# Kernel optimization log

Measured on AMD Instinct MI355X. Metric: run time of the kernel, lower is better.

The kernel has to match this reference:

```python
import jax, jax.numpy as jnp
import numpy as np


def _hilbert_d2xy(n, d):
    # standard Hilbert curve: distance d -> (x, y) on n x n grid (n power of 2)
    x = y = 0
    t = d
    s = 1
    while s < n:
        rx = 1 & (t // 2)
        ry = 1 & (t ^ rx)
        if ry == 0:
            if rx == 1:
                x = s - 1 - x
                y = s - 1 - y
            x, y = y, x
        x += s * rx
        y += s * ry
        t //= 4
        s *= 2
    return x, y


def _hilbert_perm(seq_len):
    n = int(round(np.sqrt(seq_len)))
    assert n * n == seq_len
    perm = np.empty(seq_len, dtype=np.int32)
    for d in range(seq_len):
        x, y = _hilbert_d2xy(n, d)
        perm[d] = y * n + x  # linear (row-major) index visited at Hilbert step d
    return perm


def setup_inputs() -> dict:
    key = jax.random.key(0)
    k1, k2, k3 = jax.random.split(key, 3)
    B, S, H, D = 1, 4096, 8, 64
    q = jax.random.normal(k1, (B, S, H, D), dtype=jnp.float32)
    k = jax.random.normal(k2, (B, S, H, D), dtype=jnp.float32)
    v = jax.random.normal(k3, (B, S, H, D), dtype=jnp.float32)
    hilbert_perm = jnp.asarray(_hilbert_perm(S))
    return {"q": q, "k": k, "v": v, "hilbert_perm": hilbert_perm}


def reference(q, k, v, hilbert_perm):
    B, S, H, D = q.shape
    inv_perm = jnp.argsort(hilbert_perm)

    # apply_hilbert_ordering along dim=1 (seq): gather by permutation
    q_o = q[:, hilbert_perm]
    k_o = k[:, hilbert_perm]
    v_o = v[:, hilbert_perm]

    # faithful to original: raw flat reshape of [B,S,H,D] -> [B*H, S, D]
    q_f = q_o.reshape(B * H, S, D)
    k_f = k_o.reshape(B * H, S, D)
    v_f = v_o.reshape(B * H, S, D)

    scale = 1.0 / jnp.sqrt(jnp.asarray(D, dtype=q.dtype))
    scores = jnp.einsum('bsd,btd->bst', q_f, k_f) * scale  # [B*H, S, S]
    attn = jax.nn.softmax(scores, axis=-1)
    out_f = jnp.einsum('bst,btd->bsd', attn, v_f)  # [B*H, S, D]

    out = out_f.reshape(B, H, S, D).transpose(0, 2, 1, 3).reshape(B, S, H, D)
    # inverse Hilbert ordering along dim=1
    return out[:, inv_perm]
```

## Files before the change

kernel.cpp:

```cpp
#include <hip/hip_runtime.h>

typedef _Float16 f16;
typedef _Float16 f16x4 __attribute__((ext_vector_type(4)));
typedef _Float16 f16x8 __attribute__((ext_vector_type(8)));
typedef __fp16 fp16x2 __attribute__((ext_vector_type(2)));
typedef float f32x4 __attribute__((ext_vector_type(4)));

#define MFMA_16x16x32_F16(A, B, C) __builtin_amdgcn_mfma_f32_16x16x32_f16((A), (B), (C), 0, 0, 0)

typedef const __attribute__((address_space(1))) char gchar;
typedef __attribute__((address_space(3))) char lchar;

__device__ __forceinline__ float fexp2(float x) { return __builtin_amdgcn_exp2f(x); }
__device__ __forceinline__ int swzb(int b) { return b ^ ((b >> 3) & 0x70); }

namespace {
constexpr int SB = 4096;
constexpr size_t BB = (size_t)SB * 64 * 2;
}

__device__ __forceinline__ int kinv(int r) {
    return 32 * (r >> 5) + 8 * ((r >> 2) & 3) + 4 * ((r >> 4) & 1) + (r & 3);
}

__global__ __launch_bounds__(256)
void hilbert_prepass_kernel(const float* __restrict__ kp, const float* __restrict__ vp,
                            const int* __restrict__ perm,
                            char* __restrict__ kw, char* __restrict__ vtw)
{
    const int bid = blockIdx.x;
    const int batch = bid & 7;
    const int tile = bid >> 3;
    const int tid = (int)threadIdx.x;
    const int r = tid >> 2;
    const int c4 = tid & 3;

    __shared__ float Vl[64][68];

    const int t = tile * 64 + r;
    const int srow = perm[batch * 512 + (t >> 3)];
    const size_t boff = (size_t)srow * 512 + (t & 7) * 64 + c4 * 16;

    {
        const float* ks = kp + boff;
        const float4 k0 = *(const float4*)(ks + 0);
        const float4 k1 = *(const float4*)(ks + 4);
        const float4 k2 = *(const float4*)(ks + 8);
        const float4 k3 = *(const float4*)(ks + 12);
        f16x8 h0, h1;
        h0[0] = (f16)k0.x; h0[1] = (f16)k0.y; h0[2] = (f16)k0.z; h0[3] = (f16)k0.w;
        h0[4] = (f16)k1.x; h0[5] = (f16)k1.y; h0[6] = (f16)k1.z; h0[7] = (f16)k1.w;
        h1[0] = (f16)k2.x; h1[1] = (f16)k2.y; h1[2] = (f16)k2.z; h1[3] = (f16)k2.w;
        h1[4] = (f16)k3.x; h1[5] = (f16)k3.y; h1[6] = (f16)k3.z; h1[7] = (f16)k3.w;
        char* kt = kw + (size_t)batch * BB + (size_t)tile * 8192;
        const int o = r * 128 + c4 * 32;
        *(f16x8*)(kt + swzb(o)) = h0;
        *(f16x8*)(kt + swzb(o + 16)) = h1;
    }
    {
        const float* vs = vp + boff;
        *(float4*)&Vl[r][c4 * 16 + 0]  = *(const float4*)(vs + 0);
        *(float4*)&Vl[r][c4 * 16 + 4]  = *(const float4*)(vs + 4);
        *(float4*)&Vl[r][c4 * 16 + 8]  = *(const float4*)(vs + 8);
        *(float4*)&Vl[r][c4 * 16 + 12] = *(const float4*)(vs + 12);
    }
    __syncthreads();
    {
        const int d = tid >> 2;
        const int a = tid & 3;
        char* vt = vtw + (size_t)batch * BB + (size_t)tile * 8192;
        const int b0 = 32 * (a >> 1) + 4 * (a & 1);
#pragma unroll
        for (int gp = 0; gp < 4; ++gp) {
            f16x4 qv;
#pragma unroll
            for (int v = 0; v < 4; ++v) qv[v] = (f16)Vl[16 * a + 4 * gp + v][d];
            *(f16x4*)(vt + swzb(d * 128 + (b0 + 8 * gp) * 2)) = qv;
        }
    }
}

__global__ __launch_bounds__(512, 2)
void hilbert_attn_kernel(const float* __restrict__ qp,
                         const int* __restrict__ perm,
                         const char* __restrict__ kw, const char* __restrict__ vtw,
                         float* __restrict__ op)
{
    __shared__ __align__(16) char SM[131072];

    const int bid = blockIdx.x;
    const int batch = bid & 7;
    const int qbase = (bid >> 3) * 128;
    const int tid = (int)threadIdx.x;
    const int w = tid >> 6;
    const int lane = tid & 63;
    const int l16 = lane & 15;
    const int g = lane >> 4;
    const int Kq = w >> 1;
    const int wq = w & 1;
    const int swz = (l16 & 7) << 4;

    f16x8 Qf[4][2];
    {
        constexpr float qscl = 0.125f * 1.44269504088896340736f;
#pragma unroll
        for (int s = 0; s < 4; ++s) {
            const int t = qbase + wq * 64 + s * 16 + l16;
            const int srow = perm[batch * 512 + (t >> 3)];
            const float* src = qp + (size_t)srow * 512 + (t & 7) * 64 + g * 8;
#pragma unroll
            for (int kt = 0; kt < 2; ++kt) {
                const float4 x0 = *(const float4*)(src + 32 * kt);
                const float4 x1 = *(const float4*)(src + 32 * kt + 4);
                f16x8 f;
                f[0] = (f16)(x0.x * qscl); f[1] = (f16)(x0.y * qscl);
                f[2] = (f16)(x0.z * qscl); f[3] = (f16)(x0.w * qscl);
                f[4] = (f16)(x1.x * qscl); f[5] = (f16)(x1.y * qscl);
                f[6] = (f16)(x1.z * qscl); f[7] = (f16)(x1.w * qscl);
                Qf[s][kt] = f;
            }
        }
    }

    f32x4 oacc[4][4];
#pragma unroll
    for (int s = 0; s < 4; ++s)
#pragma unroll
        for (int i = 0; i < 4; ++i) oacc[s][i] = (f32x4){0.f, 0.f, 0.f, 0.f};
    float lr[4] = {0.f, 0.f, 0.f, 0.f};

    const char* ksrc = kw + (size_t)batch * BB + (size_t)tid * 16;
    const char* vsrc = vtw + (size_t)batch * BB + (size_t)tid * 16;

    union U8 { f16x8 v; fp16x2 h[4]; };

    {
        lchar* dst = (lchar*)&SM[w << 10];
#pragma unroll
        for (int c = 0; c < 4; ++c) {
            __builtin_amdgcn_global_load_lds((gchar*)(ksrc + c * 8192), dst + c * 8192, 16, 0, 0);
            __builtin_amdgcn_global_load_lds((gchar*)(vsrc + c * 8192), dst + 32768 + c * 8192, 16, 0, 0);
        }
    }
    asm volatile("s_waitcnt vmcnt(0)" ::: "memory");
    __builtin_amdgcn_s_barrier();

    for (int it = 0; it < 15; ++it) {
        const int cur = it & 1;
        const int kbb = cur * 65536 + Kq * 8192;
        const int vbb = cur * 65536 + 32768 + Kq * 8192;
        const size_t go = (size_t)(it + 1) * 32768;
        lchar* dstb = (lchar*)&SM[(cur ^ 1) * 65536 + (w << 10)];

#pragma unroll
        for (int c = 0; c < 4; ++c)
            __builtin_amdgcn_global_load_lds((gchar*)(ksrc + go + c * 8192), dstb + c * 8192, 16, 0, 0);

        U8 Pk0[4], Pk1[4];
#pragma unroll
        for (int mt = 0; mt < 4; ++mt) {
            f32x4 sa[4];
#pragma unroll
            for (int s = 0; s < 4; ++s) sa[s] = (f32x4){0.f, 0.f, 0.f, 0.f};
            __builtin_amdgcn_s_setprio(1);
#pragma unroll
            for (int kt = 0; kt < 2; ++kt) {
                const int off = kbb + (l16 + 16 * mt) * 128 + (((g + 4 * kt) * 16) ^ swz);
                const f16x8 kf = *(const f16x8*)&SM[off];
#pragma unroll
                for (int s = 0; s < 4; ++s) sa[s] = MFMA_16x16x32_F16(kf, Qf[s][kt], sa[s]);
            }
            __builtin_amdgcn_s_setprio(0);
#pragma unroll
            for (int s = 0; s < 4; ++s) {
                const float a0 = fexp2(sa[s][0]);
                const float a1 = fexp2(sa[s][1]);
                const float a2 = fexp2(sa[s][2]);
                const float a3 = fexp2(sa[s][3]);
                lr[s] += (a0 + a1) + (a2 + a3);
                const fp16x2 h0 = __builtin_amdgcn_cvt_pkrtz(a0, a1);
                const fp16x2 h1 = __builtin_amdgcn_cvt_pkrtz(a2, a3);
                if (mt < 2) { Pk0[s].h[2 * mt] = h0; Pk0[s].h[2 * mt + 1] = h1; }
                else        { Pk1[s].h[2 * (mt - 2)] = h0; Pk1[s].h[2 * (mt - 2) + 1] = h1; }
            }
        }

#pragma unroll
        for (int c = 0; c < 4; ++c)
            __builtin_amdgcn_global_load_lds((gchar*)(vsrc + go + c * 8192), dstb + 32768 + c * 8192, 16, 0, 0);

        asm volatile("s_waitcnt vmcnt(8)" ::: "memory");
        __builtin_amdgcn_s_barrier();

        __builtin_amdgcn_s_setprio(1);
#pragma unroll
        for (int kt = 0; kt < 2; ++kt) {
#pragma unroll
            for (int mtd = 0; mtd < 4; ++mtd) {
                const int voff = vbb + (l16 + 16 * mtd) * 128 + (((g + 4 * kt) * 16) ^ swz);
                const f16x8 vf = *(const f16x8*)&SM[voff];
#pragma unroll
                for (int s = 0; s < 4; ++s)
                    oacc[s][mtd] = MFMA_16x16x32_F16(vf, kt ? Pk1[s].v : Pk0[s].v, oacc[s][mtd]);
            }
        }
        __builtin_amdgcn_s_setprio(0);

        asm volatile("s_waitcnt vmcnt(4)" ::: "memory");
        __builtin_amdgcn_s_barrier();
    }

    {
        const int kbb = 65536 + Kq * 8192;
        const int vbb = 65536 + 32768 + Kq * 8192;

        U8 Pk0[4], Pk1[4];
#pragma unroll
        for (int mt = 0; mt < 4; ++mt) {
            f32x4 sa[4];
#pragma unroll
            for (int s = 0; s < 4; ++s) sa[s] = (f32x4){0.f, 0.f, 0.f, 0.f};
#pragma unroll
            for (int kt = 0; kt < 2; ++kt) {
                const int off = kbb + (l16 + 16 * mt) * 128 + (((g + 4 * kt) * 16) ^ swz);
                const f16x8 kf = *(const f16x8*)&SM[off];
#pragma unroll
                for (int s = 0; s < 4; ++s) sa[s] = MFMA_16x16x32_F16(kf, Qf[s][kt], sa[s]);
            }
#pragma unroll
            for (int s = 0; s < 4; ++s) {
                const float a0 = fexp2(sa[s][0]);
                const float a1 = fexp2(sa[s][1]);
                const float a2 = fexp2(sa[s][2]);
                const float a3 = fexp2(sa[s][3]);
                lr[s] += (a0 + a1) + (a2 + a3);
                const fp16x2 h0 = __builtin_amdgcn_cvt_pkrtz(a0, a1);
                const fp16x2 h1 = __builtin_amdgcn_cvt_pkrtz(a2, a3);
                if (mt < 2) { Pk0[s].h[2 * mt] = h0; Pk0[s].h[2 * mt + 1] = h1; }
                else        { Pk1[s].h[2 * (mt - 2)] = h0; Pk1[s].h[2 * (mt - 2) + 1] = h1; }
            }
        }
        asm volatile("s_waitcnt vmcnt(0)" ::: "memory");
        __builtin_amdgcn_s_barrier();
#pragma unroll
        for (int kt = 0; kt < 2; ++kt) {
#pragma unroll
            for (int mtd = 0; mtd < 4; ++mtd) {
                const int voff = vbb + (l16 + 16 * mtd) * 128 + (((g + 4 * kt) * 16) ^ swz);
                const f16x8 vf = *(const f16x8*)&SM[voff];
#pragma unroll
                for (int s = 0; s < 4; ++s)
                    oacc[s][mtd] = MFMA_16x16x32_F16(vf, kt ? Pk1[s].v : Pk0[s].v, oacc[s][mtd]);
            }
        }
    }

#pragma unroll
    for (int s = 0; s < 4; ++s) {
        lr[s] += __shfl_xor(lr[s], 16);
        lr[s] += __shfl_xor(lr[s], 32);
    }

    __syncthreads();

    float* OB = (float*)SM;
    float* ML = (float*)&SM[98304];
    if (Kq >= 1) {
        float* ob = OB + ((Kq - 1) * 2 + wq) * 4096;
#pragma unroll
        for (int s = 0; s < 4; ++s)
#pragma unroll
            for (int mtd = 0; mtd < 4; ++mtd)
                *(f32x4*)&ob[(s * 16 + l16) * 64 + mtd * 16 + g * 4] = oacc[s][mtd];
        if (g == 0)
#pragma unroll
            for (int s = 0; s < 4; ++s)
                ML[((Kq - 1) * 2 + wq) * 64 + s * 16 + l16] = lr[s];
    }
    __syncthreads();
    if (Kq == 0) {
#pragma unroll
        for (int s = 0; s < 4; ++s) {
            float lsum = lr[s];
#pragma unroll
            for (int p = 0; p < 3; ++p) lsum += ML[(p * 2 + wq) * 64 + s * 16 + l16];
            const float linv = 1.f / lsum;
            const int t = qbase + wq * 64 + s * 16 + l16;
            const int srow = perm[t];
            float* dst = op + (size_t)srow * 512 + batch * 64 + 4 * g;
#pragma unroll
            for (int mtd = 0; mtd < 4; ++mtd) {
                f32x4 acc = oacc[s][mtd];
#pragma unroll
                for (int p = 0; p < 3; ++p) {
                    const f32x4 o2 = *(const f32x4*)&OB[(p * 2 + wq) * 4096 +
                                                        (s * 16 + l16) * 64 + mtd * 16 + g * 4];
                    acc[0] += o2[0]; acc[1] += o2[1]; acc[2] += o2[2]; acc[3] += o2[3];
                }
                float4 o;
                o.x = acc[0] * linv; o.y = acc[1] * linv;
                o.z = acc[2] * linv; o.w = acc[3] * linv;
                *(float4*)(dst + 16 * mtd) = o;
            }
        }
    }
}

extern "C" void kernel_launch(void* const* d_in, const int* in_sizes, int n_in,
                              void* d_out, int out_size, void* d_ws, size_t ws_size,
                              hipStream_t stream) {
    (void)in_sizes; (void)n_in; (void)out_size; (void)ws_size;
    const float* q = (const float*)d_in[0];
    const float* k = (const float*)d_in[1];
    const float* v = (const float*)d_in[2];
    const int* perm = (const int*)d_in[3];
    float* out = (float*)d_out;
    char* kw = (char*)d_ws;
    char* vtw = kw + 8 * BB;
    hipLaunchKernelGGL(hilbert_prepass_kernel, dim3(512), dim3(256), 0, stream,
                       k, v, perm, kw, vtw);
    hipLaunchKernelGGL(hilbert_attn_kernel, dim3(256), dim3(512), 0, stream,
                       q, perm, kw, vtw, out);
}
```

Measured before the change: 51.55 us.

## Give each wave private double-buffered K/V staging to drop block barriers

Each wave now streams its own 32-key group of K and V into a private double-buffered LDS slice and runs 32 smaller iterations, so the cooperative block-wide loads and the s_barrier calls inside the loop are gone. The V^T prepass layout changes to 32-key groups of 4 KB with a new XOR swizzle, and the attention kernel's V reads follow that layout. Waves no longer stall on each other, but each iteration does less MFMA work per load and wait, and the shorter loads may give less latency hiding.

```diff
diff --git a/kernel.cpp b/kernel.cpp
--- a/kernel.cpp
+++ b/kernel.cpp
@@ -19,9 +19,6 @@
 constexpr size_t BB = (size_t)SB * 64 * 2;
 }
 
-__device__ __forceinline__ int kinv(int r) {
-    return 32 * (r >> 5) + 8 * ((r >> 2) & 3) + 4 * ((r >> 4) & 1) + (r & 3);
-}
 
 __global__ __launch_bounds__(256)
 void hilbert_prepass_kernel(const float* __restrict__ kp, const float* __restrict__ vp,
@@ -68,14 +65,14 @@
     {
         const int d = tid >> 2;
         const int a = tid & 3;
-        char* vt = vtw + (size_t)batch * BB + (size_t)tile * 8192;
-        const int b0 = 32 * (a >> 1) + 4 * (a & 1);
+        char* vg = vtw + (size_t)batch * BB + ((size_t)tile * 2 + (a >> 1)) * 4096;
+        const int half8 = (a & 1) * 8;
 #pragma unroll
         for (int gp = 0; gp < 4; ++gp) {
             f16x4 qv;
 #pragma unroll
             for (int v = 0; v < 4; ++v) qv[v] = (f16)Vl[16 * a + 4 * gp + v][d];
-            *(f16x4*)(vt + swzb(d * 128 + (b0 + 8 * gp) * 2)) = qv;
+            *(f16x4*)(vg + d * 64 + ((gp ^ (d & 3)) << 4) + half8) = qv;
         }
     }
 }
@@ -98,7 +95,6 @@
     const int g = lane >> 4;
     const int Kq = w >> 1;
     const int wq = w & 1;
-    const int swz = (l16 & 7) << 4;
 
     f16x8 Qf[4][2];
     {
@@ -129,131 +125,94 @@
         for (int i = 0; i < 4; ++i) oacc[s][i] = (f32x4){0.f, 0.f, 0.f, 0.f};
     float lr[4] = {0.f, 0.f, 0.f, 0.f};
 
-    const char* ksrc = kw + (size_t)batch * BB + (size_t)tid * 16;
-    const char* vsrc = vtw + (size_t)batch * BB + (size_t)tid * 16;
+    const char* kbase = kw + (size_t)batch * BB;
+    const char* vbase = vtw + (size_t)batch * BB;
+    const int gr0 = Kq * 32;
+    lchar* myL = (lchar*)&SM[w * 16384];
 
     union U8 { f16x8 v; fp16x2 h[4]; };
 
-    {
-        lchar* dst = (lchar*)&SM[w << 10];
-#pragma unroll
-        for (int c = 0; c < 4; ++c) {
-            __builtin_amdgcn_global_load_lds((gchar*)(ksrc + c * 8192), dst + c * 8192, 16, 0, 0);
-            __builtin_amdgcn_global_load_lds((gchar*)(vsrc + c * 8192), dst + 32768 + c * 8192, 16, 0, 0);
-        }
-    }
+#define STAGE_GR(buf, gr)                                                            \
+    do {                                                                             \
+        lchar* dst_ = myL + (buf) * 8192;                                            \
+        const char* ks_ = kbase + ((gr) >> 1) * 8192 + ((gr) & 1) * 4096 + lane * 16;\
+        const char* vs_ = vbase + (size_t)(gr) * 4096 + lane * 16;                   \
+        __builtin_amdgcn_global_load_lds((gchar*)(ks_ + 0),    dst_ + 0,    16, 0, 0);\
+        __builtin_amdgcn_global_load_lds((gchar*)(ks_ + 1024), dst_ + 1024, 16, 0, 0);\
+        __builtin_amdgcn_global_load_lds((gchar*)(ks_ + 2048), dst_ + 2048, 16, 0, 0);\
+        __builtin_amdgcn_global_load_lds((gchar*)(ks_ + 3072), dst_ + 3072, 16, 0, 0);\
+        __builtin_amdgcn_global_load_lds((gchar*)(vs_ + 0),    dst_ + 4096, 16, 0, 0);\
+        __builtin_amdgcn_global_load_lds((gchar*)(vs_ + 1024), dst_ + 5120, 16, 0, 0);\
+        __builtin_amdgcn_global_load_lds((gchar*)(vs_ + 2048), dst_ + 6144, 16, 0, 0);\
+        __builtin_amdgcn_global_load_lds((gchar*)(vs_ + 3072), dst_ + 7168, 16, 0, 0);\
+    } while (0)
+
+    STAGE_GR(0, gr0);
     asm volatile("s_waitcnt vmcnt(0)" ::: "memory");
-    __builtin_amdgcn_s_barrier();
-
-    for (int it = 0; it < 15; ++it) {
-        const int cur = it & 1;
-        const int kbb = cur * 65536 + Kq * 8192;
-        const int vbb = cur * 65536 + 32768 + Kq * 8192;
-        const size_t go = (size_t)(it + 1) * 32768;
-        lchar* dstb = (lchar*)&SM[(cur ^ 1) * 65536 + (w << 10)];
-
-#pragma unroll
-        for (int c = 0; c < 4; ++c)
-            __builtin_amdgcn_global_load_lds((gchar*)(ksrc + go + c * 8192), dstb + c * 8192, 16, 0, 0);
-
-        U8 Pk0[4], Pk1[4];
-#pragma unroll
-        for (int mt = 0; mt < 4; ++mt) {
-            f32x4 sa[4];
-#pragma unroll
-            for (int s = 0; s < 4; ++s) sa[s] = (f32x4){0.f, 0.f, 0.f, 0.f};
-            __builtin_amdgcn_s_setprio(1);
-#pragma unroll
-            for (int kt = 0; kt < 2; ++kt) {
-                const int off = kbb + (l16 + 16 * mt) * 128 + (((g + 4 * kt) * 16) ^ swz);
-                const f16x8 kf = *(const f16x8*)&SM[off];
-#pragma unroll
-                for (int s = 0; s < 4; ++s) sa[s] = MFMA_16x16x32_F16(kf, Qf[s][kt], sa[s]);
-            }
-            __builtin_amdgcn_s_setprio(0);
-#pragma unroll
-            for (int s = 0; s < 4; ++s) {
-                const float a0 = fexp2(sa[s][0]);
-                const float a1 = fexp2(sa[s][1]);
-                const float a2 = fexp2(sa[s][2]);
-                const float a3 = fexp2(sa[s][3]);
+
+    for (int it = 0; it < 32; ++it) {
+        const int buf = it & 1;
+        if (it < 31) {
+            STAGE_GR(buf ^ 1, gr0 + it + 1);
+            asm volatile("s_waitcnt vmcnt(8)" ::: "memory");
+        } else {
+            asm volatile("s_waitcnt vmcnt(0)" ::: "memory");
+        }
+        const char* Kl = (const char*)&SM[w * 16384 + buf * 8192];
+
+        f16x8 kf[4], vf[4];
+#pragma unroll
+        for (int kt = 0; kt < 2; ++kt)
+#pragma unroll
+            for (int mt = 0; mt < 2; ++mt) {
+                const int off = (l16 + 16 * mt) * 128 + (((g + 4 * kt) * 16) ^ ((l16 & 7) << 4));
+                kf[kt * 2 + mt] = *(const f16x8*)&Kl[off];
+            }
+#pragma unroll
+        for (int mtd = 0; mtd < 4; ++mtd) {
+            const int voff = 4096 + (l16 + 16 * mtd) * 64 + ((g ^ (l16 & 3)) << 4);
+            vf[mtd] = *(const f16x8*)&Kl[voff];
+        }
+
+        f32x4 sa[4][2];
+#pragma unroll
+        for (int s = 0; s < 4; ++s)
+#pragma unroll
+            for (int mt = 0; mt < 2; ++mt) sa[s][mt] = (f32x4){0.f, 0.f, 0.f, 0.f};
+        __builtin_amdgcn_s_setprio(1);
+#pragma unroll
+        for (int kt = 0; kt < 2; ++kt)
+#pragma unroll
+            for (int mt = 0; mt < 2; ++mt)
+#pragma unroll
+                for (int s = 0; s < 4; ++s)
+                    sa[s][mt] = MFMA_16x16x32_F16(kf[kt * 2 + mt], Qf[s][kt], sa[s][mt]);
+        __builtin_amdgcn_s_setprio(0);
+
+        U8 P[4];
+#pragma unroll
+        for (int s = 0; s < 4; ++s) {
+#pragma unroll
+            for (int mt = 0; mt < 2; ++mt) {
+                const float a0 = fexp2(sa[s][mt][0]);
+                const float a1 = fexp2(sa[s][mt][1]);
+                const float a2 = fexp2(sa[s][mt][2]);
+                const float a3 = fexp2(sa[s][mt][3]);
                 lr[s] += (a0 + a1) + (a2 + a3);
-                const fp16x2 h0 = __builtin_amdgcn_cvt_pkrtz(a0, a1);
-                const fp16x2 h1 = __builtin_amdgcn_cvt_pkrtz(a2, a3);
-                if (mt < 2) { Pk0[s].h[2 * mt] = h0; Pk0[s].h[2 * mt + 1] = h1; }
-                else        { Pk1[s].h[2 * (mt - 2)] = h0; Pk1[s].h[2 * (mt - 2) + 1] = h1; }
-            }
-        }
-
-#pragma unroll
-        for (int c = 0; c < 4; ++c)
-            __builtin_amdgcn_global_load_lds((gchar*)(vsrc + go + c * 8192), dstb + 32768 + c * 8192, 16, 0, 0);
-
-        asm volatile("s_waitcnt vmcnt(8)" ::: "memory");
-        __builtin_amdgcn_s_barrier();
+                P[s].h[2 * mt]     = __builtin_amdgcn_cvt_pkrtz(a0, a1);
+                P[s].h[2 * mt + 1] = __builtin_amdgcn_cvt_pkrtz(a2, a3);
+            }
+        }
 
         __builtin_amdgcn_s_setprio(1);
 #pragma unroll
-        for (int kt = 0; kt < 2; ++kt) {
-#pragma unroll
-            for (int mtd = 0; mtd < 4; ++mtd) {
-                const int voff = vbb + (l16 + 16 * mtd) * 128 + (((g + 4 * kt) * 16) ^ swz);
-                const f16x8 vf = *(const f16x8*)&SM[voff];
-#pragma unroll
-                for (int s = 0; s < 4; ++s)
-                    oacc[s][mtd] = MFMA_16x16x32_F16(vf, kt ? Pk1[s].v : Pk0[s].v, oacc[s][mtd]);
-            }
-        }
+        for (int mtd = 0; mtd < 4; ++mtd)
+#pragma unroll
+            for (int s = 0; s < 4; ++s)
+                oacc[s][mtd] = MFMA_16x16x32_F16(vf[mtd], P[s].v, oacc[s][mtd]);
         __builtin_amdgcn_s_setprio(0);
-
-        asm volatile("s_waitcnt vmcnt(4)" ::: "memory");
-        __builtin_amdgcn_s_barrier();
-    }
-
-    {
-        const int kbb = 65536 + Kq * 8192;
-        const int vbb = 65536 + 32768 + Kq * 8192;
-
-        U8 Pk0[4], Pk1[4];
-#pragma unroll
-        for (int mt = 0; mt < 4; ++mt) {
-            f32x4 sa[4];
-#pragma unroll
-            for (int s = 0; s < 4; ++s) sa[s] = (f32x4){0.f, 0.f, 0.f, 0.f};
-#pragma unroll
-            for (int kt = 0; kt < 2; ++kt) {
-                const int off = kbb + (l16 + 16 * mt) * 128 + (((g + 4 * kt) * 16) ^ swz);
-                const f16x8 kf = *(const f16x8*)&SM[off];
-#pragma unroll
-                for (int s = 0; s < 4; ++s) sa[s] = MFMA_16x16x32_F16(kf, Qf[s][kt], sa[s]);
-            }
-#pragma unroll
-            for (int s = 0; s < 4; ++s) {
-                const float a0 = fexp2(sa[s][0]);
-                const float a1 = fexp2(sa[s][1]);
-                const float a2 = fexp2(sa[s][2]);
-                const float a3 = fexp2(sa[s][3]);
-                lr[s] += (a0 + a1) + (a2 + a3);
-                const fp16x2 h0 = __builtin_amdgcn_cvt_pkrtz(a0, a1);
-                const fp16x2 h1 = __builtin_amdgcn_cvt_pkrtz(a2, a3);
-                if (mt < 2) { Pk0[s].h[2 * mt] = h0; Pk0[s].h[2 * mt + 1] = h1; }
-                else        { Pk1[s].h[2 * (mt - 2)] = h0; Pk1[s].h[2 * (mt - 2) + 1] = h1; }
-            }
-        }
-        asm volatile("s_waitcnt vmcnt(0)" ::: "memory");
-        __builtin_amdgcn_s_barrier();
-#pragma unroll
-        for (int kt = 0; kt < 2; ++kt) {
-#pragma unroll
-            for (int mtd = 0; mtd < 4; ++mtd) {
-                const int voff = vbb + (l16 + 16 * mtd) * 128 + (((g + 4 * kt) * 16) ^ swz);
-                const f16x8 vf = *(const f16x8*)&SM[voff];
-#pragma unroll
-                for (int s = 0; s < 4; ++s)
-                    oacc[s][mtd] = MFMA_16x16x32_F16(vf, kt ? Pk1[s].v : Pk0[s].v, oacc[s][mtd]);
-            }
-        }
-    }
+    }
+#undef STAGE_GR
 
 #pragma unroll
     for (int s = 0; s < 4; ++s) {
```

After: 54.34 us. 1.05x slower.
